# Kernel optimization log

Hardware: AMD Instinct MI355X
Metric: run time of the kernel (lower is better)

## Reference

```python
import jax, jax.numpy as jnp
import numpy as np

RHO = 1.0


def _cayley():
    # Geometric-product structure constants for Cl(2,0), basis (1, e1, e2, e12).
    C = np.zeros((4, 4, 4), dtype=np.float32)
    entries = [
        (0, 0, 0, 1), (0, 1, 1, 1), (0, 2, 2, 1), (0, 3, 3, 1),
        (1, 0, 1, 1), (1, 1, 0, 1), (1, 2, 3, 1), (1, 3, 2, 1),
        (2, 0, 2, 1), (2, 1, 3, -1), (2, 2, 0, 1), (2, 3, 1, -1),
        (3, 0, 3, 1), (3, 1, 2, -1), (3, 2, 1, 1), (3, 3, 0, -1),
    ]
    for x, y, z, s in entries:
        C[x, y, z] = s
    return jnp.asarray(C)

CAYLEY = _cayley()

B, I, O, G, X = 64, 64, 64, 4096, 4
GRID_MIN, GRID_MAX = -2.0, 2.0


def setup_inputs() -> dict:
    key = jax.random.key(0)
    k1, k2, k3 = jax.random.split(key, 3)
    x = jax.random.normal(k1, (B, I, X), dtype=jnp.float32)
    # random_grid: quasirandom points in [grid_min, grid_max]^X (Sobol in torch; uniform here)
    grid = jax.random.uniform(k2, (G, X), dtype=jnp.float32) * (GRID_MAX - GRID_MIN) + GRID_MIN
    weights = jax.random.normal(k3, (I, O, G, X), dtype=jnp.float32)
    silu_weight = jnp.ones((I, O, X), dtype=jnp.float32)
    silu_bias = jnp.zeros((I, O, X), dtype=jnp.float32)
    return {"x": x, "grid": grid, "weights": weights,
            "silu_weight": silu_weight, "silu_bias": silu_bias}


def reference(x, grid, weights, silu_weight, silu_bias):
    # x: (B, I, X); grid: (G, X); weights: (I, O, G, X)
    diff = x[:, :, None, :] - grid[None, None, :, :]          # (B, I, G, X)
    # algebra.norm(v)**2 with Euclidean metric = sum over multivector components
    rbf = jnp.exp(-jnp.sum(diff * diff, axis=-1) / RHO)       # (B, I, G)
    result = jnp.einsum('big,iogx->biox', rbf, weights)       # (B, I, O, X)
    # componentwise SiLU branch: geometric product via cayley tensor
    sx = jax.nn.silu(x)                                       # (B, I, X)
    silu_val = jnp.einsum('iox,biy,xyz->bioz', silu_weight, sx, CAYLEY)
    silu_val = silu_val + silu_bias                           # broadcast (B, I, O, X)
    out = jnp.sum(result + silu_val, axis=1)                  # 'biox->box'
    return out                                                # NoNorm: identity norm
```

## Files before the change

### kernel.cpp

```cpp
#include <hip/hip_runtime.h>
#include <hip/hip_bf16.h>

#define BB 64
#define II 64
#define OO 64
#define GG 4096
#define KP 64
#define NPH 16
#define NSL 512

typedef short bf16x8 __attribute__((ext_vector_type(8)));
typedef float f32x4  __attribute__((ext_vector_type(4)));
typedef unsigned short u16x4 __attribute__((ext_vector_type(4)));

static __device__ __forceinline__ short f2bf(float f) {
    __hip_bfloat16 h = __float2bfloat16(f);
    return __builtin_bit_cast(short, h);
}
static __device__ __forceinline__ unsigned short f2bfu(float f) {
    __hip_bfloat16 h = __float2bfloat16(f);
    return __builtin_bit_cast(unsigned short, h);
}
static __device__ __forceinline__ float bfu2f(unsigned short u) {
    unsigned int v = (unsigned int)u << 16;
    return __builtin_bit_cast(float, v);
}

__global__ __launch_bounds__(512, 4)
void kan_main(const float* __restrict__ xg, const float* __restrict__ grd,
              const float* __restrict__ wts, unsigned short* __restrict__ dst,
              float* __restrict__ fdst, int atomic_mode)
{
    __shared__ __align__(16) float          Wst[2][32 * 256];
    __shared__ __align__(16) unsigned short As [BB * KP];
    __shared__ __align__(16) float4         Gs [KP];

    const int i   = blockIdx.x;
    const int oc  = blockIdx.y;
    const int gch = blockIdx.z;
    const int s   = (i + 4 * gch + 8 * oc) & (NPH - 1);

    const int t    = threadIdx.x;
    const int lane = t & 63;
    const int wv   = t >> 6;

    const int brow = t >> 3;
    const int oct  = t & 7;
    const float4 xv = reinterpret_cast<const float4*>(xg)[brow * II + i];

    const float4* w4 = reinterpret_cast<const float4*>(wts)
        + ((size_t)i * OO + oc * 32) * GG + (size_t)gch * 1024;
    const float4* g4 = reinterpret_cast<const float4*>(grd) + gch * 1024;
    const int qs_hi = (lane >> 3) & 1;

    __builtin_amdgcn_global_load_lds(g4 + s * KP + lane, (char*)(&Gs[0]),
                                     16, 0, 0);
    #pragma unroll
    for (int q = 0; q < 4; ++q) {
        const int rr = q * 8 + wv;
        const int qs = ((rr & 3) << 1) | qs_hi;
        __builtin_amdgcn_global_load_lds(
            w4 + (size_t)rr * GG + s * KP + (lane ^ qs),
            (char*)(&Wst[0][0]) + rr * 1024, 16, 0, 0);
    }
    asm volatile("s_waitcnt vmcnt(4)" ::: "memory");

    {
        bf16x8 pa;
        #pragma unroll
        for (int e = 0; e < 8; ++e) {
            const float4 g = Gs[oct * 8 + e];
            const float d0 = xv.x - g.x, d1 = xv.y - g.y,
                        d2 = xv.z - g.z, d3 = xv.w - g.w;
            pa[e] = f2bf(__expf(-(d0*d0 + d1*d1 + d2*d2 + d3*d3)));
        }
        *reinterpret_cast<bf16x8*>(
            &As[brow * KP + ((oct * 8) ^ ((brow & 7) << 3))]) = pa;
    }
    asm volatile("s_waitcnt lgkmcnt(0)\n\ts_barrier" ::: "memory");
    __builtin_amdgcn_global_load_lds(g4 + ((s + 1) & (NPH - 1)) * KP + lane,
                                     (char*)(&Gs[0]), 16, 0, 0);

    f32x4 acc[4];
    #pragma unroll
    for (int mt = 0; mt < 4; ++mt) acc[mt] = {0.f, 0.f, 0.f, 0.f};

    const int lg   = lane >> 4;
    const int r16  = lane & 15;
    const int orow = wv * 4 + (r16 >> 2);
    const int bx   = r16 & 3;

    for (int p = 0; p < NPH; ++p) {
        const int b  = p & 1;
        const int cp = (p + s) & (NPH - 1);
        const int np = (p + 1 + s) & (NPH - 1);

        if (p + 1 < NPH) {
            #pragma unroll
            for (int q = 0; q < 4; ++q) {
                const int rr = q * 8 + wv;
                const int qs = ((rr & 3) << 1) | qs_hi;
                __builtin_amdgcn_global_load_lds(
                    w4 + (size_t)rr * GG + np * KP + (lane ^ qs),
                    (char*)(&Wst[b ^ 1][0]) + rr * 1024, 16, 0, 0);
            }
        }

        if (p + 1 < NPH)
            asm volatile("s_waitcnt vmcnt(4)" ::: "memory");
        else
            asm volatile("s_waitcnt vmcnt(0)" ::: "memory");

        bf16x8 pa;
        if (p + 1 < NPH) {
            #pragma unroll
            for (int e = 0; e < 8; ++e) {
                const float4 g = Gs[oct * 8 + e];
                const float d0 = xv.x - g.x, d1 = xv.y - g.y,
                            d2 = xv.z - g.z, d3 = xv.w - g.w;
                pa[e] = f2bf(__expf(-(d0*d0 + d1*d1 + d2*d2 + d3*d3)));
            }
        }

        asm volatile("s_waitcnt lgkmcnt(0)\n\ts_barrier" ::: "memory");

        #pragma unroll
        for (int kk = 0; kk < 2; ++kk) {
            bf16x8 bb;
            #pragma unroll
            for (int e = 0; e < 8; ++e) {
                const int g  = kk * 32 + lg * 8 + e;
                const int qp = ((orow & 3) << 1) | (lg & 1);
                bb[e] = f2bf(Wst[b][orow * 256 + ((g ^ qp) << 2) + bx]);
            }
            #pragma unroll
            for (int mt = 0; mt < 4; ++mt) {
                const int rA = mt * 16 + r16;
                const bf16x8 af = *reinterpret_cast<const bf16x8*>(
                    &As[rA * KP + ((kk * 32 + lg * 8) ^ ((rA & 7) << 3))]);
                acc[mt] = __builtin_amdgcn_mfma_f32_16x16x32_bf16(
                    af, bb, acc[mt], 0, 0, 0);
            }
        }

        asm volatile("s_waitcnt lgkmcnt(0)\n\ts_barrier" ::: "memory");

        if (p + 1 < NPH) {
            *reinterpret_cast<bf16x8*>(
                &As[brow * KP + ((oct * 8) ^ ((brow & 7) << 3))]) = pa;
        }
        if (p + 2 < NPH) {
            __builtin_amdgcn_global_load_lds(
                g4 + ((p + 2 + s) & (NPH - 1)) * KP + lane,
                (char*)(&Gs[0]), 16, 0, 0);
        }
    }

    const int nloc = wv * 16 + r16;
    const int mb   = ((lane >> 4) << 2);
    if (!atomic_mode) {
        unsigned short* pd = dst
            + (size_t)((i * 2 + oc) * 4 + gch) * (BB * 128);
        #pragma unroll
        for (int mt = 0; mt < 4; ++mt)
            #pragma unroll
            for (int r = 0; r < 4; ++r)
                pd[(mt * 16 + mb + r) * 128 + nloc] = f2bfu(acc[mt][r]);
    } else {
        #pragma unroll
        for (int mt = 0; mt < 4; ++mt)
            #pragma unroll
            for (int r = 0; r < 4; ++r)
                atomicAdd(&fdst[(mt * 16 + mb + r) * 256 + oc * 128 + nloc],
                          acc[mt][r]);
    }
}

__global__ __launch_bounds__(256)
void kan_tail(const unsigned short* __restrict__ part,
              const float* __restrict__ xg,
              const float* __restrict__ sw,
              const float* __restrict__ sb,
              float* __restrict__ out)
{
    __shared__ float4 sums[16][16];

    const int t     = threadIdx.x;
    const int bid   = blockIdx.x;
    const int pairL = t & 15;
    const int rgrp  = t >> 4;
    const int pairG = bid * 16 + pairL;
    const int b     = pairG >> 6, o = pairG & 63;
    const int oc    = o >> 5;

    float4 s4 = make_float4(0.f, 0.f, 0.f, 0.f);
    #pragma unroll 4
    for (int m = 0; m < 16; ++m) {
        const int idx = rgrp * 16 + m;
        const int ii  = idx >> 2, gg = idx & 3;
        const size_t sl = (size_t)((ii * 2 + oc) * 4 + gg);
        const u16x4 v = *reinterpret_cast<const u16x4*>(
            part + sl * (BB * 128) + b * 128 + (o & 31) * 4);
        s4.x += bfu2f(v[0]); s4.y += bfu2f(v[1]);
        s4.z += bfu2f(v[2]); s4.w += bfu2f(v[3]);
    }
    sums[pairL][rgrp] = s4;
    __syncthreads();

    if (t < 16) {
        const int pg = bid * 16 + t;
        const int bb = pg >> 6, oo = pg & 63;

        float o0 = 0.f, o1 = 0.f, o2 = 0.f, o3 = 0.f;
        #pragma unroll
        for (int r = 0; r < 16; ++r) {
            const float4 v = sums[t][r];
            o0 += v.x; o1 += v.y; o2 += v.z; o3 += v.w;
        }

        const float4* xg4 = reinterpret_cast<const float4*>(xg);
        const float4* sw4 = reinterpret_cast<const float4*>(sw);
        const float4* sb4 = reinterpret_cast<const float4*>(sb);
        #pragma unroll 4
        for (int i = 0; i < II; ++i) {
            const float4 xvv = xg4[bb * II + i];
            const float4 swv = sw4[i * OO + oo];
            const float4 sbv = sb4[i * OO + oo];
            const float s0 = xvv.x / (1.f + __expf(-xvv.x));
            const float s1 = xvv.y / (1.f + __expf(-xvv.y));
            const float s2 = xvv.z / (1.f + __expf(-xvv.z));
            const float s3 = xvv.w / (1.f + __expf(-xvv.w));
            o0 += swv.x * s0 + swv.y * s1 + swv.z * s2 - swv.w * s3 + sbv.x;
            o1 += swv.x * s1 + swv.y * s0 - swv.z * s3 + swv.w * s2 + sbv.y;
            o2 += swv.x * s2 + swv.y * s3 + swv.z * s0 - swv.w * s1 + sbv.z;
            o3 += swv.x * s3 + swv.y * s2 - swv.z * s1 + swv.w * s0 + sbv.w;
        }
        reinterpret_cast<float4*>(out)[pg] = make_float4(o0, o1, o2, o3);
    }
}

__global__ void kan_out(const float* __restrict__ xg,
                        const float* __restrict__ sw,
                        const float* __restrict__ sb,
                        float* __restrict__ out)
{
    const int t = blockIdx.x * 256 + threadIdx.x;
    const int b = t >> 6, o = t & 63;

    const float4 v = reinterpret_cast<const float4*>(out)[t];
    float o0 = v.x, o1 = v.y, o2 = v.z, o3 = v.w;

    const float4* xg4 = reinterpret_cast<const float4*>(xg);
    const float4* sw4 = reinterpret_cast<const float4*>(sw);
    const float4* sb4 = reinterpret_cast<const float4*>(sb);
    #pragma unroll 4
    for (int i = 0; i < II; ++i) {
        const float4 xvv = xg4[b * II + i];
        const float4 swv = sw4[i * OO + o];
        const float4 sbv = sb4[i * OO + o];
        const float s0 = xvv.x / (1.f + __expf(-xvv.x));
        const float s1 = xvv.y / (1.f + __expf(-xvv.y));
        const float s2 = xvv.z / (1.f + __expf(-xvv.z));
        const float s3 = xvv.w / (1.f + __expf(-xvv.w));
        o0 += swv.x * s0 + swv.y * s1 + swv.z * s2 - swv.w * s3 + sbv.x;
        o1 += swv.x * s1 + swv.y * s0 - swv.z * s3 + swv.w * s2 + sbv.y;
        o2 += swv.x * s2 + swv.y * s3 + swv.z * s0 - swv.w * s1 + sbv.z;
        o3 += swv.x * s3 + swv.y * s2 - swv.z * s1 + swv.w * s0 + sbv.w;
    }
    reinterpret_cast<float4*>(out)[t] = make_float4(o0, o1, o2, o3);
}

extern "C" void kernel_launch(void* const* d_in, const int* in_sizes, int n_in,
                              void* d_out, int out_size, void* d_ws, size_t ws_size,
                              hipStream_t stream)
{
    const float* x   = (const float*)d_in[0];
    const float* grd = (const float*)d_in[1];
    const float* w   = (const float*)d_in[2];
    const float* sw  = (const float*)d_in[3];
    const float* sb  = (const float*)d_in[4];
    float* out = (float*)d_out;

    const size_t need = (size_t)NSL * (BB * 128) * 2;

    if (ws_size >= need) {
        unsigned short* ws = (unsigned short*)d_ws;
        kan_main<<<dim3(64, 2, 4), 512, 0, stream>>>(x, grd, w, ws, nullptr, 0);
        kan_tail<<<256, 256, 0, stream>>>(ws, x, sw, sb, out);
    } else {
        hipMemsetAsync(d_out, 0, (size_t)out_size * sizeof(float), stream);
        kan_main<<<dim3(64, 2, 4), 512, 0, stream>>>(x, grd, w, nullptr, out, 1);
        kan_out<<<16, 256, 0, stream>>>(x, sw, sb, out);
    }
}
```

Baseline: 70.59 us.

## Retile main kernel to 16 outputs per block and longer grid phases

```diff
diff --git a/kernel.cpp b/kernel.cpp
--- a/kernel.cpp
+++ b/kernel.cpp
@@ -6,7 +6,7 @@
 #define OO 64
 #define GG 4096
 #define KP 64
-#define NPH 16
+#define NPH 32
 #define NSL 512
 
 typedef short bf16x8 __attribute__((ext_vector_type(8)));
@@ -31,14 +31,14 @@
               const float* __restrict__ wts, unsigned short* __restrict__ dst,
               float* __restrict__ fdst, int atomic_mode)
 {
-    __shared__ __align__(16) float          Wst[2][32 * 256];
+    __shared__ __align__(16) float          Wst[2][16 * 256];
     __shared__ __align__(16) unsigned short As [BB * KP];
     __shared__ __align__(16) float4         Gs [KP];
 
     const int i   = blockIdx.x;
     const int oc  = blockIdx.y;
     const int gch = blockIdx.z;
-    const int s   = (i + 4 * gch + 8 * oc) & (NPH - 1);
+    const int s   = (i + 8 * oc + 16 * gch) & (NPH - 1);
 
     const int t    = threadIdx.x;
     const int lane = t & 63;
@@ -49,21 +49,21 @@
     const float4 xv = reinterpret_cast<const float4*>(xg)[brow * II + i];
 
     const float4* w4 = reinterpret_cast<const float4*>(wts)
-        + ((size_t)i * OO + oc * 32) * GG + (size_t)gch * 1024;
-    const float4* g4 = reinterpret_cast<const float4*>(grd) + gch * 1024;
+        + ((size_t)i * OO + oc * 16) * GG + (size_t)gch * 2048;
+    const float4* g4 = reinterpret_cast<const float4*>(grd) + gch * 2048;
     const int qs_hi = (lane >> 3) & 1;
 
     __builtin_amdgcn_global_load_lds(g4 + s * KP + lane, (char*)(&Gs[0]),
                                      16, 0, 0);
     #pragma unroll
-    for (int q = 0; q < 4; ++q) {
+    for (int q = 0; q < 2; ++q) {
         const int rr = q * 8 + wv;
         const int qs = ((rr & 3) << 1) | qs_hi;
         __builtin_amdgcn_global_load_lds(
             w4 + (size_t)rr * GG + s * KP + (lane ^ qs),
             (char*)(&Wst[0][0]) + rr * 1024, 16, 0, 0);
     }
-    asm volatile("s_waitcnt vmcnt(4)" ::: "memory");
+    asm volatile("s_waitcnt vmcnt(2)" ::: "memory");
 
     {
         bf16x8 pa;
@@ -81,23 +81,23 @@
     __builtin_amdgcn_global_load_lds(g4 + ((s + 1) & (NPH - 1)) * KP + lane,
                                      (char*)(&Gs[0]), 16, 0, 0);
 
-    f32x4 acc[4];
-    #pragma unroll
-    for (int mt = 0; mt < 4; ++mt) acc[mt] = {0.f, 0.f, 0.f, 0.f};
+    f32x4 acc[2];
+    acc[0] = {0.f, 0.f, 0.f, 0.f};
+    acc[1] = {0.f, 0.f, 0.f, 0.f};
 
     const int lg   = lane >> 4;
     const int r16  = lane & 15;
-    const int orow = wv * 4 + (r16 >> 2);
+    const int mt   = wv & 3;
+    const int ntg  = wv >> 2;
     const int bx   = r16 & 3;
 
     for (int p = 0; p < NPH; ++p) {
         const int b  = p & 1;
-        const int cp = (p + s) & (NPH - 1);
         const int np = (p + 1 + s) & (NPH - 1);
 
         if (p + 1 < NPH) {
             #pragma unroll
-            for (int q = 0; q < 4; ++q) {
+            for (int q = 0; q < 2; ++q) {
                 const int rr = q * 8 + wv;
                 const int qs = ((rr & 3) << 1) | qs_hi;
                 __builtin_amdgcn_global_load_lds(
@@ -107,7 +107,7 @@
         }
 
         if (p + 1 < NPH)
-            asm volatile("s_waitcnt vmcnt(4)" ::: "memory");
+            asm volatile("s_waitcnt vmcnt(2)" ::: "memory");
         else
             asm volatile("s_waitcnt vmcnt(0)" ::: "memory");
 
@@ -126,20 +126,22 @@
 
         #pragma unroll
         for (int kk = 0; kk < 2; ++kk) {
-            bf16x8 bb;
-            #pragma unroll
-            for (int e = 0; e < 8; ++e) {
-                const int g  = kk * 32 + lg * 8 + e;
-                const int qp = ((orow & 3) << 1) | (lg & 1);
-                bb[e] = f2bf(Wst[b][orow * 256 + ((g ^ qp) << 2) + bx]);
-            }
-            #pragma unroll
-            for (int mt = 0; mt < 4; ++mt) {
-                const int rA = mt * 16 + r16;
-                const bf16x8 af = *reinterpret_cast<const bf16x8*>(
-                    &As[rA * KP + ((kk * 32 + lg * 8) ^ ((rA & 7) << 3))]);
-                acc[mt] = __builtin_amdgcn_mfma_f32_16x16x32_bf16(
-                    af, bb, acc[mt], 0, 0, 0);
+            const int rA = mt * 16 + r16;
+            const bf16x8 af = *reinterpret_cast<const bf16x8*>(
+                &As[rA * KP + ((kk * 32 + lg * 8) ^ ((rA & 7) << 3))]);
+            #pragma unroll
+            for (int nn = 0; nn < 2; ++nn) {
+                const int nt   = ntg * 2 + nn;
+                const int orow = nt * 4 + (r16 >> 2);
+                const int qp   = ((orow & 3) << 1) | (lg & 1);
+                bf16x8 bb;
+                #pragma unroll
+                for (int e = 0; e < 8; ++e) {
+                    const int g = kk * 32 + lg * 8 + e;
+                    bb[e] = f2bf(Wst[b][orow * 256 + ((g ^ qp) << 2) + bx]);
+                }
+                acc[nn] = __builtin_amdgcn_mfma_f32_16x16x32_bf16(
+                    af, bb, acc[nn], 0, 0, 0);
             }
         }
 
@@ -156,23 +158,25 @@
         }
     }
 
-    const int nloc = wv * 16 + r16;
-    const int mb   = ((lane >> 4) << 2);
+    const int mb = mt * 16 + ((lane >> 4) << 2);
     if (!atomic_mode) {
         unsigned short* pd = dst
-            + (size_t)((i * 2 + oc) * 4 + gch) * (BB * 128);
-        #pragma unroll
-        for (int mt = 0; mt < 4; ++mt)
+            + (size_t)((i * 4 + oc) * 2 + gch) * (BB * 64);
+        #pragma unroll
+        for (int nn = 0; nn < 2; ++nn) {
+            const int n = (ntg * 2 + nn) * 16 + r16;
             #pragma unroll
             for (int r = 0; r < 4; ++r)
-                pd[(mt * 16 + mb + r) * 128 + nloc] = f2bfu(acc[mt][r]);
+                pd[(mb + r) * 64 + n] = f2bfu(acc[nn][r]);
+        }
     } else {
         #pragma unroll
-        for (int mt = 0; mt < 4; ++mt)
+        for (int nn = 0; nn < 2; ++nn) {
+            const int n = oc * 64 + (ntg * 2 + nn) * 16 + r16;
             #pragma unroll
             for (int r = 0; r < 4; ++r)
-                atomicAdd(&fdst[(mt * 16 + mb + r) * 256 + oc * 128 + nloc],
-                          acc[mt][r]);
+                atomicAdd(&fdst[(mb + r) * 256 + n], acc[nn][r]);
+        }
     }
 }
 
@@ -191,16 +195,17 @@
     const int rgrp  = t >> 4;
     const int pairG = bid * 16 + pairL;
     const int b     = pairG >> 6, o = pairG & 63;
-    const int oc    = o >> 5;
+    const int oc    = o >> 4;
+    const int ncol  = (o & 15) * 4;
 
     float4 s4 = make_float4(0.f, 0.f, 0.f, 0.f);
     #pragma unroll 4
-    for (int m = 0; m < 16; ++m) {
-        const int idx = rgrp * 16 + m;
-        const int ii  = idx >> 2, gg = idx & 3;
-        const size_t sl = (size_t)((ii * 2 + oc) * 4 + gg);
+    for (int m = 0; m < 8; ++m) {
+        const int idx = rgrp * 8 + m;
+        const int ii  = idx >> 1, gg = idx & 1;
+        const size_t sl = (size_t)((ii * 4 + oc) * 2 + gg);
         const u16x4 v = *reinterpret_cast<const u16x4*>(
-            part + sl * (BB * 128) + b * 128 + (o & 31) * 4);
+            part + sl * (BB * 64) + b * 64 + ncol);
         s4.x += bfu2f(v[0]); s4.y += bfu2f(v[1]);
         s4.z += bfu2f(v[2]); s4.w += bfu2f(v[3]);
     }
@@ -281,15 +286,15 @@
     const float* sb  = (const float*)d_in[4];
     float* out = (float*)d_out;
 
-    const size_t need = (size_t)NSL * (BB * 128) * 2;
+    const size_t need = (size_t)NSL * (BB * 64) * 2;
 
     if (ws_size >= need) {
         unsigned short* ws = (unsigned short*)d_ws;
-        kan_main<<<dim3(64, 2, 4), 512, 0, stream>>>(x, grd, w, ws, nullptr, 0);
+        kan_main<<<dim3(64, 4, 2), 512, 0, stream>>>(x, grd, w, ws, nullptr, 0);
         kan_tail<<<256, 256, 0, stream>>>(ws, x, sw, sb, out);
     } else {
         hipMemsetAsync(d_out, 0, (size_t)out_size * sizeof(float), stream);
-        kan_main<<<dim3(64, 2, 4), 512, 0, stream>>>(x, grd, w, nullptr, out, 1);
+        kan_main<<<dim3(64, 4, 2), 512, 0, stream>>>(x, grd, w, nullptr, out, 1);
         kan_out<<<16, 256, 0, stream>>>(x, sw, sb, out);
     }
 }
```

Result: slower. 107.8 us (+52.7%).
